# Kernel tuning notes

Hardware: AMD Instinct MI355X
Metric: run time of the kernel (lower is better)

Reference implementation:

```python
import jax, jax.numpy as jnp
import numpy as np

N = 4096        # number of nodes
C = 512         # in_features
L_LAT = 64      # L_latent
EPS = 0.25      # epsilon


def setup_inputs() -> dict:
    key = jax.random.key(0)
    ks = jax.random.split(key, 8)
    def lin(k, fan_in, shape):
        return (jax.random.normal(k, shape, jnp.float32) / np.float32(np.sqrt(fan_in)))
    x = jax.random.normal(ks[0], (N, C), jnp.float32)
    adj = jax.random.uniform(ks[1], (N, N), jnp.float32)  # dense nonneg kernel
    W_proj = lin(ks[2], C, (C, L_LAT)); b_proj = jnp.zeros((L_LAT,), jnp.float32)
    W_pi1 = lin(ks[3], L_LAT, (L_LAT, C)); b_pi1 = jnp.zeros((C,), jnp.float32)
    W_pi2 = lin(ks[4], C, (C, 1)); b_pi2 = jnp.zeros((1,), jnp.float32)
    W_f = lin(ks[5], C, (C, C)); b_f = jnp.zeros((C,), jnp.float32)
    dt = jnp.array([0.1], jnp.float32)
    return {"x": x, "adj": adj, "W_proj": W_proj, "b_proj": b_proj,
            "W_pi1": W_pi1, "b_pi1": b_pi1, "W_pi2": W_pi2, "b_pi2": b_pi2,
            "W_f": W_f, "b_f": b_f, "dt": dt}


def reference(x, adj, W_proj, b_proj, W_pi1, b_pi1, W_pi2, b_pi2, W_f, b_f, dt):
    # proj_list: x -> latent [n, L]
    z = x @ W_proj + b_proj
    # pi_list: Linear -> ReLU -> Linear -> Sigmoid, squeeze to [n]
    pi = jax.nn.sigmoid(jax.nn.relu(z @ W_pi1 + b_pi1) @ W_pi2 + b_pi2)[:, 0]
    # q_epsilon_tilde: row sums of the kernel
    q = adj.sum(axis=1)                       # [n]
    # K_tilde = K_epsilon @ diag(pi/q)  == column scaling
    K_tilde = adj * (pi / q)[None, :]         # [n, n]
    # D_tilde diagonal; torch.inverse of a diagonal == elementwise reciprocal
    d = K_tilde.sum(axis=1) + 1e-5            # [n]
    # target = relu(f(x)) with f = Linear(C, C)
    target = jax.nn.relu(x @ W_f + b_f)       # [n, C]
    # L @ target = (1/eps) * diag(1/d) @ K_tilde @ target - target
    Lt = (K_tilde @ target) / (EPS * d)[:, None] - target
    return target + dt[0] * Lt
```

## Files before the change

kernel.cpp:

```cpp
#include <hip/hip_runtime.h>
#include <hip/hip_bf16.h>

#define N_NODES 4096
#define C_DIM   512
#define L_DIM   64
#define SPLITS  4
#define KCHUNK  (N_NODES / SPLITS)

typedef unsigned short u16;
using bf16x8 = __attribute__((ext_vector_type(8))) __bf16;
using u16x8  = __attribute__((ext_vector_type(8))) unsigned short;
using f32x4  = __attribute__((ext_vector_type(4))) float;

__device__ __forceinline__ float b2f(u16 u) {
    union { unsigned int i; float f; } v; v.i = ((unsigned int)u) << 16; return v.f;
}
__device__ __forceinline__ u16 f2b(float f) {
    unsigned int u = __float_as_uint(f);
    u += 0x7fff + ((u >> 16) & 1);
    return (u16)(u >> 16);
}

__device__ __forceinline__ void gload16(const u16* g, u16* l) {
    __builtin_amdgcn_global_load_lds((const __attribute__((address_space(1))) void*)g,
                                     (__attribute__((address_space(3))) void*)l,
                                     16, 0, 0);
}

__device__ __forceinline__ int detect_mode_inl(const u16* __restrict__ adj) {
    int m = 0;
#pragma unroll
    for (int i = 0; i < 64; ++i) m |= (adj[i] >= 0x8000) ? 1 : 0;
    return m;
}

#define OFF_DT    64
#define OFF_BIAS  1024
#define OFF_WP    4096
#define OFF_BP    135168
#define OFF_WP1   135424
#define OFF_BP1   266496
#define OFF_WP2   268544
#define OFF_BP2   270592
#define OFF_Q     271360
#define OFF_S     287744
#define OFF_DV    304128
#define OFF_T     1048576
#define OFF_TST   9437184
#define OFF_WFT   13631488
#define OFF_XB    14155776
#define OFF_ADJB  18350080

__device__ __forceinline__ float ldin(const void* p, int i, int mode) {
    if (mode) return ((const float*)p)[i];
    return b2f(((const u16*)p)[i]);
}

__global__ __launch_bounds__(256) void k1_prep(const void* __restrict__ adj, const void* __restrict__ x,
        const void* Wp, const void* bp, const void* Wp1, const void* bp1,
        const void* Wp2, const void* bp2, const void* Wf, const void* bfc, const void* dt,
        float* __restrict__ Wp_f, float* __restrict__ bp_f, float* __restrict__ Wp1_f,
        float* __restrict__ bp1_f, float* __restrict__ Wp2_f, float* __restrict__ bp2_f,
        float* __restrict__ bias_f, float* __restrict__ dt_f,
        u16* __restrict__ adjb, float* __restrict__ q, u16* __restrict__ xb,
        u16* __restrict__ WfT) {
    __shared__ float tile[32][33];
    int bid = blockIdx.x, tid = threadIdx.x;
    int mode = detect_mode_inl((const u16*)adj);
    if (bid < 263) {
        int idx = bid * 256 + tid;
        if (idx < 32768)        Wp_f[idx]          = ldin(Wp,  idx, mode);
        else if (idx < 32832)   bp_f[idx - 32768]  = ldin(bp,  idx - 32768, mode);
        else if (idx < 65600)   Wp1_f[idx - 32832] = ldin(Wp1, idx - 32832, mode);
        else if (idx < 66112)   bp1_f[idx - 65600] = ldin(bp1, idx - 65600, mode);
        else if (idx < 66624)   Wp2_f[idx - 66112] = ldin(Wp2, idx - 66112, mode);
        else if (idx == 66624)  bp2_f[0]           = ldin(bp2, 0, mode);
        else if (idx < 67137)   bias_f[idx - 66625] = ldin(bfc, idx - 66625, mode);
        else if (idx == 67137)  dt_f[0]            = ldin(dt, 0, mode);
    } else if (bid < 2311) {
        if (mode == 0) return;
        int idx = (bid - 263) * 256 + tid;
        float4 v = ((const float4*)x)[idx];
        ushort4 o; o.x = f2b(v.x); o.y = f2b(v.y); o.z = f2b(v.z); o.w = f2b(v.w);
        ((ushort4*)xb)[idx] = o;
    } else if (bid < 3335) {
        int wave = tid >> 6, lane = tid & 63;
        int row = (bid - 2311) * 4 + wave;
        float acc = 0.f;
        if (mode) {
            const float4* rp = (const float4*)((const float*)adj + (size_t)row * N_NODES);
            ushort4* wp = (ushort4*)(adjb + (size_t)row * N_NODES);
#pragma unroll
            for (int it = 0; it < 16; ++it) {
                float4 v = rp[it * 64 + lane];
                acc += v.x + v.y + v.z + v.w;
                ushort4 o; o.x = f2b(v.x); o.y = f2b(v.y); o.z = f2b(v.z); o.w = f2b(v.w);
                wp[it * 64 + lane] = o;
            }
        } else {
            const u16x8* rp = (const u16x8*)((const u16*)adj + (size_t)row * N_NODES);
#pragma unroll
            for (int it = 0; it < 8; ++it) {
                u16x8 v = rp[it * 64 + lane];
#pragma unroll
                for (int e = 0; e < 8; ++e) acc += b2f(v[e]);
            }
        }
#pragma unroll
        for (int off = 32; off > 0; off >>= 1) acc += __shfl_down(acc, off);
        if (lane == 0) q[row] = acc;
    } else {
        int g = bid - 3335;
        int tx = tid & 31, ty = tid >> 5;
        int x0 = (g & 15) * 32, y0 = (g >> 4) * 32;
        if (mode) {
            const float* src = (const float*)Wf;
#pragma unroll
            for (int r = ty; r < 32; r += 8) tile[r][tx] = src[(size_t)(y0 + r) * C_DIM + x0 + tx];
        } else {
            const u16* src = (const u16*)Wf;
#pragma unroll
            for (int r = ty; r < 32; r += 8) tile[r][tx] = b2f(src[(size_t)(y0 + r) * C_DIM + x0 + tx]);
        }
        __syncthreads();
#pragma unroll
        for (int r = ty; r < 32; r += 8)
            WfT[(size_t)(x0 + r) * C_DIM + y0 + tx] = f2b(tile[tx][r]);
    }
}

__global__ __launch_bounds__(256) void k2_pi_gemm1(const void* __restrict__ xraw,
        const u16* __restrict__ adjdet, const u16* __restrict__ xb, const u16* __restrict__ WfT,
        const float* __restrict__ Wp_f,  const float* __restrict__ bp_f,
        const float* __restrict__ Wp1_f, const float* __restrict__ bp1_f,
        const float* __restrict__ Wp2_f, const float* __restrict__ bp2_f,
        const float* __restrict__ bias_f, const float* __restrict__ dt_f,
        const float* __restrict__ q, float* __restrict__ s, float* __restrict__ T,
        void* __restrict__ out, float* __restrict__ Pacc) {
    __shared__ __align__(16) char smem[18560];
    int bid = blockIdx.x, tid = threadIdx.x;
    int mode = detect_mode_inl(adjdet);
    if (bid < 512) {
        float (*sx)[C_DIM] = (float(*)[C_DIM])smem;
        float (*sz)[L_DIM] = (float(*)[L_DIM])(smem + 16384);
        float (*red)[8]    = (float(*)[8])(smem + 18432);
        int i0 = bid * 8;
        const u16* xsrc = mode ? xb : (const u16*)xraw;
        const u16x8* xp = (const u16x8*)(xsrc + (size_t)i0 * C_DIM);
#pragma unroll
        for (int r = 0; r < 2; ++r) {
            u16x8 v = xp[tid + 256 * r];
            float* dstf = &sx[0][0] + (size_t)(tid + 256 * r) * 8;
#pragma unroll
            for (int e = 0; e < 8; ++e) dstf[e] = b2f(v[e]);
        }
        __syncthreads();
        int j = tid & 63, n0 = tid >> 6;
        float a0 = 0.f, a1 = 0.f;
#pragma unroll 4
        for (int k = 0; k < C_DIM; ++k) {
            float w = Wp_f[k * L_DIM + j];
            a0 += sx[n0][k] * w;
            a1 += sx[n0 + 4][k] * w;
        }
        sz[n0][j] = a0 + bp_f[j];
        sz[n0 + 4][j] = a1 + bp_f[j];
        __syncthreads();
        int m0 = tid, m1 = tid + 256;
        float b0 = bp1_f[m0], b1 = bp1_f[m1];
        float h0[8], h1[8];
#pragma unroll
        for (int n = 0; n < 8; ++n) { h0[n] = b0; h1[n] = b1; }
#pragma unroll 8
        for (int jj = 0; jj < L_DIM; ++jj) {
            float w0 = Wp1_f[jj * C_DIM + m0];
            float w1 = Wp1_f[jj * C_DIM + m1];
#pragma unroll
            for (int n = 0; n < 8; ++n) {
                float z = sz[n][jj];
                h0[n] += z * w0;
                h1[n] += z * w1;
            }
        }
        float w2a = Wp2_f[m0], w2b = Wp2_f[m1];
        float p[8];
#pragma unroll
        for (int n = 0; n < 8; ++n)
            p[n] = fmaxf(h0[n], 0.f) * w2a + fmaxf(h1[n], 0.f) * w2b;
#pragma unroll
        for (int off = 32; off > 0; off >>= 1)
#pragma unroll
            for (int n = 0; n < 8; ++n) p[n] += __shfl_down(p[n], off);
        int lane = tid & 63, wave = tid >> 6;
        if (lane == 0) {
#pragma unroll
            for (int n = 0; n < 8; ++n) red[wave][n] = p[n];
        }
        __syncthreads();
        if (tid < 8) {
            float tot = red[0][tid] + red[1][tid] + red[2][tid] + red[3][tid] + bp2_f[0];
            float pi = 1.f / (1.f + expf(-tot));
            s[i0 + tid] = pi / q[i0 + tid];
        }
    } else {
        u16* lA = (u16*)smem;
        u16* lB = (u16*)(smem + 4096);
        const u16* A = mode ? xb : (const u16*)xraw;
        float* tgt = mode ? (float*)out : Pacc;
        int g = bid - 512;
        int lane = tid & 63, wave = tid >> 6;
        int bm = (g & 63) * 64, bn = (g >> 6) * 64;
        int quad = lane >> 4, l15 = lane & 15;
        int wm = wave * 16;
        const u16* Ap = A + (size_t)(bm + (tid >> 2)) * C_DIM + (tid & 3) * 8;
        const u16* Bp = WfT + (size_t)(bn + (tid >> 2)) * C_DIM + (tid & 3) * 8;
        u16* la = lA + tid * 8;
        u16* lb = lB + tid * 8;
        f32x4 acc[4];
#pragma unroll
        for (int nt = 0; nt < 4; ++nt) acc[nt] = (f32x4){0.f, 0.f, 0.f, 0.f};
        for (int k0 = 0; k0 < C_DIM; k0 += 32) {
            gload16(Ap + k0, la);
            gload16(Bp + k0, lb);
            __syncthreads();
            bf16x8 af = *(const bf16x8*)&lA[(wm + l15) * 32 + quad * 8];
            bf16x8 bfv[4];
#pragma unroll
            for (int nt = 0; nt < 4; ++nt) bfv[nt] = *(const bf16x8*)&lB[(nt * 16 + l15) * 32 + quad * 8];
#pragma unroll
            for (int nt = 0; nt < 4; ++nt)
                acc[nt] = __builtin_amdgcn_mfma_f32_16x16x32_bf16(af, bfv[nt], acc[nt], 0, 0, 0);
            __syncthreads();
        }
        float c0 = 1.f - dt_f[0];
#pragma unroll
        for (int nt = 0; nt < 4; ++nt) {
            int col = bn + nt * 16 + l15;
            float bv = bias_f[col];
#pragma unroll
            for (int r = 0; r < 4; ++r) {
                int row = bm + wm + quad * 4 + r;
                float t = fmaxf(acc[nt][r] + bv, 0.f);
                T[(size_t)row * C_DIM + col] = t;
                tgt[(size_t)row * C_DIM + col] = c0 * t;
            }
        }
    }
}

__global__ __launch_bounds__(256) void k3_mid(const void* __restrict__ adjraw,
        const u16* __restrict__ adjb, const float* __restrict__ s,
        const float* __restrict__ T,
        float* __restrict__ dv, u16* __restrict__ TsT) {
    __shared__ float tile[32][33];
    int bid = blockIdx.x, tid = threadIdx.x;
    int mode = detect_mode_inl((const u16*)adjraw);
    if (bid < 1024) {
        const u16* A = mode ? adjb : (const u16*)adjraw;
        int wave = tid >> 6, lane = tid & 63;
        int row = bid * 4 + wave;
        const u16x8* rp = (const u16x8*)(A + (size_t)row * N_NODES);
        float acc = 0.f;
#pragma unroll
        for (int it = 0; it < 8; ++it) {
            int chunk = it * 64 + lane;
            u16x8 v = rp[chunk];
            const float4* sp = (const float4*)(s + chunk * 8);
            float4 s0 = sp[0], s1 = sp[1];
            acc += b2f(v[0]) * s0.x + b2f(v[1]) * s0.y + b2f(v[2]) * s0.z + b2f(v[3]) * s0.w;
            acc += b2f(v[4]) * s1.x + b2f(v[5]) * s1.y + b2f(v[6]) * s1.z + b2f(v[7]) * s1.w;
        }
#pragma unroll
        for (int off = 32; off > 0; off >>= 1) acc += __shfl_down(acc, off);
        if (lane == 0) dv[row] = acc + 1e-5f;
    } else {
        int g = bid - 1024;
        int tx = tid & 31, ty = tid >> 5;
        int x0 = (g & 15) * 32, y0 = (g >> 4) * 32;
#pragma unroll
        for (int r = ty; r < 32; r += 8) tile[r][tx] = T[(size_t)(y0 + r) * C_DIM + x0 + tx];
        __syncthreads();
        float sv = s[y0 + tx];
#pragma unroll
        for (int r = ty; r < 32; r += 8)
            TsT[(size_t)(x0 + r) * N_NODES + y0 + tx] = f2b(tile[tx][r] * sv);
    }
}

__global__ __launch_bounds__(256) void k4_gemm2(const void* __restrict__ adjraw,
        const u16* __restrict__ adjb, const u16* __restrict__ TsT,
        const float* __restrict__ dv, const float* __restrict__ dt_f,
        void* __restrict__ out, float* __restrict__ Pacc) {
    __shared__ __align__(16) u16 lA[8192];
    __shared__ __align__(16) u16 lB[8192];
    int mode = detect_mode_inl((const u16*)adjraw);
    const u16* A = mode ? adjb : (const u16*)adjraw;
    float* tgt = mode ? (float*)out : Pacc;
    int tid = threadIdx.x;
    int lane = tid & 63, wave = tid >> 6;
    int bm = blockIdx.x * 128, bn = blockIdx.y * 128;
    int kbase = blockIdx.z * KCHUNK;
    int wm = (wave & 1) * 64, wn = (wave >> 1) * 64;
    int quad = lane >> 4, l15 = lane & 15;

    const u16* Ab0 = A + (size_t)(bm + (tid >> 2)) * N_NODES + kbase + (tid & 3) * 8;
    const u16* Ab1 = A + (size_t)(bm + 64 + (tid >> 2)) * N_NODES + kbase + (tid & 3) * 8;
    const u16* Bb0 = TsT + (size_t)(bn + (tid >> 2)) * N_NODES + kbase + (tid & 3) * 8;
    const u16* Bb1 = TsT + (size_t)(bn + 64 + (tid >> 2)) * N_NODES + kbase + (tid & 3) * 8;
    u16* la00 = lA + tid * 8;        u16* la01 = lA + 2048 + tid * 8;
    u16* la10 = lA + 4096 + tid * 8; u16* la11 = lA + 6144 + tid * 8;
    u16* lb00 = lB + tid * 8;        u16* lb01 = lB + 2048 + tid * 8;
    u16* lb10 = lB + 4096 + tid * 8; u16* lb11 = lB + 6144 + tid * 8;

    f32x4 acc[4][4];
#pragma unroll
    for (int a = 0; a < 4; ++a)
#pragma unroll
        for (int b = 0; b < 4; ++b) acc[a][b] = (f32x4){0.f, 0.f, 0.f, 0.f};

    for (int k0 = 0; k0 < KCHUNK; k0 += 64) {
        gload16(Ab0 + k0, la00);
        gload16(Ab1 + k0, la01);
        gload16(Ab0 + k0 + 32, la10);
        gload16(Ab1 + k0 + 32, la11);
        gload16(Bb0 + k0, lb00);
        gload16(Bb1 + k0, lb01);
        gload16(Bb0 + k0 + 32, lb10);
        gload16(Bb1 + k0 + 32, lb11);
        __syncthreads();
#pragma unroll
        for (int kk = 0; kk < 2; ++kk) {
            const u16* baseA = lA + kk * 4096;
            const u16* baseB = lB + kk * 4096;
            bf16x8 af[4], bfv[4];
#pragma unroll
            for (int mt = 0; mt < 4; ++mt) af[mt] = *(const bf16x8*)&baseA[(wm + mt * 16 + l15) * 32 + quad * 8];
#pragma unroll
            for (int nt = 0; nt < 4; ++nt) bfv[nt] = *(const bf16x8*)&baseB[(wn + nt * 16 + l15) * 32 + quad * 8];
#pragma unroll
            for (int mt = 0; mt < 4; ++mt)
#pragma unroll
                for (int nt = 0; nt < 4; ++nt)
                    acc[mt][nt] = __builtin_amdgcn_mfma_f32_16x16x32_bf16(af[mt], bfv[nt], acc[mt][nt], 0, 0, 0);
        }
        __syncthreads();
    }

    float c1 = dt_f[0] * 4.f;
#pragma unroll
    for (int mt = 0; mt < 4; ++mt) {
        float inv[4];
#pragma unroll
        for (int r = 0; r < 4; ++r) inv[r] = c1 / dv[bm + wm + mt * 16 + quad * 4 + r];
#pragma unroll
        for (int nt = 0; nt < 4; ++nt) {
            int col = bn + wn + nt * 16 + l15;
#pragma unroll
            for (int r = 0; r < 4; ++r) {
                int row = bm + wm + mt * 16 + quad * 4 + r;
                atomicAdd(&tgt[(size_t)row * C_DIM + col], acc[mt][nt][r] * inv[r]);
            }
        }
    }
}

__global__ __launch_bounds__(256) void k5_fin(const void* __restrict__ adjraw,
                                              const float* __restrict__ Pacc,
                                              u16* __restrict__ out) {
    if (detect_mode_inl((const u16*)adjraw)) return;
    int idx = blockIdx.x * 256 + threadIdx.x;
    float4 v = ((const float4*)Pacc)[idx];
    ushort4 o; o.x = f2b(v.x); o.y = f2b(v.y); o.z = f2b(v.z); o.w = f2b(v.w);
    ((ushort4*)out)[idx] = o;
}

extern "C" void kernel_launch(void* const* d_in, const int* in_sizes, int n_in,
                              void* d_out, int out_size, void* d_ws, size_t ws_size,
                              hipStream_t stream) {
    const void* x   = d_in[0];
    const void* adj = d_in[1];
    const void* Wp  = d_in[2];
    const void* bp  = d_in[3];
    const void* Wp1 = d_in[4];
    const void* bp1 = d_in[5];
    const void* Wp2 = d_in[6];
    const void* bp2 = d_in[7];
    const void* Wf  = d_in[8];
    const void* bfc = d_in[9];
    const void* dtp = d_in[10];
    const u16* adjdet = (const u16*)adj;

    char* ws = (char*)d_ws;
    float* dt_f   = (float*)(ws + OFF_DT);
    float* bias_f = (float*)(ws + OFF_BIAS);
    float* Wp_f   = (float*)(ws + OFF_WP);
    float* bp_f   = (float*)(ws + OFF_BP);
    float* Wp1_f  = (float*)(ws + OFF_WP1);
    float* bp1_f  = (float*)(ws + OFF_BP1);
    float* Wp2_f  = (float*)(ws + OFF_WP2);
    float* bp2_f  = (float*)(ws + OFF_BP2);
    float* q      = (float*)(ws + OFF_Q);
    float* s      = (float*)(ws + OFF_S);
    float* dv     = (float*)(ws + OFF_DV);
    float* T      = (float*)(ws + OFF_T);
    u16*   TsT    = (u16*)(ws + OFF_TST);
    u16*   WfT    = (u16*)(ws + OFF_WFT);
    u16*   xb     = (u16*)(ws + OFF_XB);
    u16*   adjb   = (u16*)(ws + OFF_ADJB);
    float* Pacc   = (float*)(ws + OFF_ADJB);

    k1_prep<<<3591, 256, 0, stream>>>(adj, x, Wp, bp, Wp1, bp1, Wp2, bp2, Wf, bfc, dtp,
                                      Wp_f, bp_f, Wp1_f, bp1_f, Wp2_f, bp2_f, bias_f, dt_f,
                                      adjb, q, xb, WfT);
    k2_pi_gemm1<<<1024, 256, 0, stream>>>(x, adjdet, xb, WfT,
                                          Wp_f, bp_f, Wp1_f, bp1_f, Wp2_f, bp2_f, bias_f, dt_f,
                                          q, s, T, d_out, Pacc);
    k3_mid<<<3072, 256, 0, stream>>>(adj, adjb, s, T, dv, TsT);
    k4_gemm2<<<dim3(32, 4, SPLITS), 256, 0, stream>>>(adj, adjb, TsT, dv, dt_f, d_out, Pacc);
    k5_fin<<<2048, 256, 0, stream>>>(adj, Pacc, (u16*)d_out);
}
```

Before: 227.5 us.

## Pack pi-MLP weights as bf16 pairs and restructure the latent projection loop

Wp and Wp1 are now converted in the prep kernel to packed bf16 pairs instead of fp32 copies, halving the weight traffic of the pi MLP. The latent projection now splits K across the four waves, with each thread computing all 8 rows, and reduces the partial sums through shared memory. The mode flag is computed once and stored in the workspace, so later kernels read one int instead of each re-scanning 64 adjacency values. The cost is bf16 rounding of the MLP weights, which could shift pi slightly, plus extra shared memory and a barrier in the MLP block.

```diff
diff --git a/kernel.cpp b/kernel.cpp
--- a/kernel.cpp
+++ b/kernel.cpp
@@ -8,6 +8,7 @@
 #define KCHUNK  (N_NODES / SPLITS)
 
 typedef unsigned short u16;
+typedef unsigned int   u32;
 using bf16x8 = __attribute__((ext_vector_type(8))) __bf16;
 using u16x8  = __attribute__((ext_vector_type(8))) unsigned short;
 using f32x4  = __attribute__((ext_vector_type(4))) float;
@@ -20,13 +21,11 @@
     u += 0x7fff + ((u >> 16) & 1);
     return (u16)(u >> 16);
 }
-
-__device__ __forceinline__ void gload16(const u16* g, u16* l) {
+__device__ __forceinline__ void gload16(const void* g, void* l) {
     __builtin_amdgcn_global_load_lds((const __attribute__((address_space(1))) void*)g,
                                      (__attribute__((address_space(3))) void*)l,
                                      16, 0, 0);
 }
-
 __device__ __forceinline__ int detect_mode_inl(const u16* __restrict__ adj) {
     int m = 0;
 #pragma unroll
@@ -34,22 +33,23 @@
     return m;
 }
 
+#define OFF_MODE  0
 #define OFF_DT    64
 #define OFF_BIAS  1024
-#define OFF_WP    4096
-#define OFF_BP    135168
-#define OFF_WP1   135424
-#define OFF_BP1   266496
-#define OFF_WP2   268544
-#define OFF_BP2   270592
-#define OFF_Q     271360
-#define OFF_S     287744
-#define OFF_DV    304128
+#define OFF_BP    4096
+#define OFF_BP1   4608
+#define OFF_WP2   8192
+#define OFF_BP2   10240
+#define OFF_Q     16384
+#define OFF_S     32768
+#define OFF_DV    49152
+#define OFF_WPP   65536
+#define OFF_WP1P  131072
+#define OFF_WFT   196608
 #define OFF_T     1048576
 #define OFF_TST   9437184
-#define OFF_WFT   13631488
-#define OFF_XB    14155776
-#define OFF_ADJB  18350080
+#define OFF_XB    13631488
+#define OFF_ADJB  17825792
 
 __device__ __forceinline__ float ldin(const void* p, int i, int mode) {
     if (mode) return ((const float*)p)[i];
@@ -59,33 +59,34 @@
 __global__ __launch_bounds__(256) void k1_prep(const void* __restrict__ adj, const void* __restrict__ x,
         const void* Wp, const void* bp, const void* Wp1, const void* bp1,
         const void* Wp2, const void* bp2, const void* Wf, const void* bfc, const void* dt,
-        float* __restrict__ Wp_f, float* __restrict__ bp_f, float* __restrict__ Wp1_f,
-        float* __restrict__ bp1_f, float* __restrict__ Wp2_f, float* __restrict__ bp2_f,
+        int* __restrict__ modep,
+        float* __restrict__ bp_f, float* __restrict__ bp1_f,
+        float* __restrict__ Wp2_f, float* __restrict__ bp2_f,
         float* __restrict__ bias_f, float* __restrict__ dt_f,
+        u32* __restrict__ WpP, u32* __restrict__ Wp1P,
         u16* __restrict__ adjb, float* __restrict__ q, u16* __restrict__ xb,
         u16* __restrict__ WfT) {
     __shared__ float tile[32][33];
     int bid = blockIdx.x, tid = threadIdx.x;
     int mode = detect_mode_inl((const u16*)adj);
-    if (bid < 263) {
+    if (bid < 7) {
+        if (bid == 0 && tid == 0) *modep = mode;
         int idx = bid * 256 + tid;
-        if (idx < 32768)        Wp_f[idx]          = ldin(Wp,  idx, mode);
-        else if (idx < 32832)   bp_f[idx - 32768]  = ldin(bp,  idx - 32768, mode);
-        else if (idx < 65600)   Wp1_f[idx - 32832] = ldin(Wp1, idx - 32832, mode);
-        else if (idx < 66112)   bp1_f[idx - 65600] = ldin(bp1, idx - 65600, mode);
-        else if (idx < 66624)   Wp2_f[idx - 66112] = ldin(Wp2, idx - 66112, mode);
-        else if (idx == 66624)  bp2_f[0]           = ldin(bp2, 0, mode);
-        else if (idx < 67137)   bias_f[idx - 66625] = ldin(bfc, idx - 66625, mode);
-        else if (idx == 67137)  dt_f[0]            = ldin(dt, 0, mode);
-    } else if (bid < 2311) {
+        if (idx < 64)           bp_f[idx]          = ldin(bp,  idx, mode);
+        else if (idx < 576)     bp1_f[idx - 64]    = ldin(bp1, idx - 64, mode);
+        else if (idx < 1088)    Wp2_f[idx - 576]   = ldin(Wp2, idx - 576, mode);
+        else if (idx == 1088)   bp2_f[0]           = ldin(bp2, 0, mode);
+        else if (idx < 1601)    bias_f[idx - 1089] = ldin(bfc, idx - 1089, mode);
+        else if (idx == 1601)   dt_f[0]            = ldin(dt, 0, mode);
+    } else if (bid < 2055) {
         if (mode == 0) return;
-        int idx = (bid - 263) * 256 + tid;
+        int idx = (bid - 7) * 256 + tid;
         float4 v = ((const float4*)x)[idx];
         ushort4 o; o.x = f2b(v.x); o.y = f2b(v.y); o.z = f2b(v.z); o.w = f2b(v.w);
         ((ushort4*)xb)[idx] = o;
-    } else if (bid < 3335) {
+    } else if (bid < 3079) {
         int wave = tid >> 6, lane = tid & 63;
-        int row = (bid - 2311) * 4 + wave;
+        int row = (bid - 2055) * 4 + wave;
         float acc = 0.f;
         if (mode) {
             const float4* rp = (const float4*)((const float*)adj + (size_t)row * N_NODES);
@@ -109,8 +110,8 @@
 #pragma unroll
         for (int off = 32; off > 0; off >>= 1) acc += __shfl_down(acc, off);
         if (lane == 0) q[row] = acc;
-    } else {
-        int g = bid - 3335;
+    } else if (bid < 3335) {
+        int g = bid - 3079;
         int tx = tid & 31, ty = tid >> 5;
         int x0 = (g & 15) * 32, y0 = (g >> 4) * 32;
         if (mode) {
@@ -126,24 +127,37 @@
 #pragma unroll
         for (int r = ty; r < 32; r += 8)
             WfT[(size_t)(x0 + r) * C_DIM + y0 + tx] = f2b(tile[tx][r]);
+    } else if (bid < 3399) {
+        int idx = (bid - 3335) * 256 + tid;
+        int k2i = idx >> 6, j = idx & 63;
+        float a = ldin(Wp, (2 * k2i) * L_DIM + j, mode);
+        float b = ldin(Wp, (2 * k2i + 1) * L_DIM + j, mode);
+        WpP[idx] = (u32)f2b(a) | ((u32)f2b(b) << 16);
+    } else {
+        int idx = (bid - 3399) * 256 + tid;
+        int jj2 = idx >> 9, m = idx & 511;
+        float a = ldin(Wp1, (2 * jj2) * C_DIM + m, mode);
+        float b = ldin(Wp1, (2 * jj2 + 1) * C_DIM + m, mode);
+        Wp1P[idx] = (u32)f2b(a) | ((u32)f2b(b) << 16);
     }
 }
 
 __global__ __launch_bounds__(256) void k2_pi_gemm1(const void* __restrict__ xraw,
-        const u16* __restrict__ adjdet, const u16* __restrict__ xb, const u16* __restrict__ WfT,
-        const float* __restrict__ Wp_f,  const float* __restrict__ bp_f,
-        const float* __restrict__ Wp1_f, const float* __restrict__ bp1_f,
+        const int* __restrict__ modep, const u16* __restrict__ xb, const u16* __restrict__ WfT,
+        const u32* __restrict__ WpP, const u32* __restrict__ Wp1P,
+        const float* __restrict__ bp_f,  const float* __restrict__ bp1_f,
         const float* __restrict__ Wp2_f, const float* __restrict__ bp2_f,
         const float* __restrict__ bias_f, const float* __restrict__ dt_f,
         const float* __restrict__ q, float* __restrict__ s, float* __restrict__ T,
         void* __restrict__ out, float* __restrict__ Pacc) {
-    __shared__ __align__(16) char smem[18560];
+    __shared__ __align__(16) char smem[26880];
     int bid = blockIdx.x, tid = threadIdx.x;
-    int mode = detect_mode_inl(adjdet);
+    int mode = *modep;
     if (bid < 512) {
-        float (*sx)[C_DIM] = (float(*)[C_DIM])smem;
-        float (*sz)[L_DIM] = (float(*)[L_DIM])(smem + 16384);
-        float (*red)[8]    = (float(*)[8])(smem + 18432);
+        float (*sx)[C_DIM]      = (float(*)[C_DIM])smem;
+        float (*red)[8][L_DIM]  = (float(*)[8][L_DIM])(smem + 16384);
+        float (*sz)[L_DIM]      = (float(*)[L_DIM])(smem + 24576);
+        float (*rw)[8]          = (float(*)[8])(smem + 26624);
         int i0 = bid * 8;
         const u16* xsrc = mode ? xb : (const u16*)xraw;
         const u16x8* xp = (const u16x8*)(xsrc + (size_t)i0 * C_DIM);
@@ -155,31 +169,44 @@
             for (int e = 0; e < 8; ++e) dstf[e] = b2f(v[e]);
         }
         __syncthreads();
-        int j = tid & 63, n0 = tid >> 6;
-        float a0 = 0.f, a1 = 0.f;
+        int j = tid & 63, part = tid >> 6;
+        float za[8];
+#pragma unroll
+        for (int n = 0; n < 8; ++n) za[n] = 0.f;
+        const u32* wp = WpP + part * 4096 + j;
+#pragma unroll 8
+        for (int kk = 0; kk < 64; ++kk) {
+            u32 w = wp[kk * 64];
+            float wa = b2f((u16)(w & 0xFFFF)), wb = b2f((u16)(w >> 16));
+            int k = part * 128 + kk * 2;
+#pragma unroll
+            for (int n = 0; n < 8; ++n) za[n] += sx[n][k] * wa + sx[n][k + 1] * wb;
+        }
+#pragma unroll
+        for (int n = 0; n < 8; ++n) red[part][n][j] = za[n];
+        __syncthreads();
+#pragma unroll
+        for (int r = 0; r < 2; ++r) {
+            int idx = tid + r * 256; int n = idx >> 6, jj = idx & 63;
+            sz[n][jj] = red[0][n][jj] + red[1][n][jj] + red[2][n][jj] + red[3][n][jj] + bp_f[jj];
+        }
+        __syncthreads();
+        int m0 = tid, m1 = tid + 256;
+        float h0[8], h1[8];
+        float b0 = bp1_f[m0], b1 = bp1_f[m1];
+#pragma unroll
+        for (int n = 0; n < 8; ++n) { h0[n] = b0; h1[n] = b1; }
+        const u32* w1p = Wp1P + m0;
 #pragma unroll 4
-        for (int k = 0; k < C_DIM; ++k) {
-            float w = Wp_f[k * L_DIM + j];
-            a0 += sx[n0][k] * w;
-            a1 += sx[n0 + 4][k] * w;
-        }
-        sz[n0][j] = a0 + bp_f[j];
-        sz[n0 + 4][j] = a1 + bp_f[j];
-        __syncthreads();
-        int m0 = tid, m1 = tid + 256;
-        float b0 = bp1_f[m0], b1 = bp1_f[m1];
-        float h0[8], h1[8];
-#pragma unroll
-        for (int n = 0; n < 8; ++n) { h0[n] = b0; h1[n] = b1; }
-#pragma unroll 8
-        for (int jj = 0; jj < L_DIM; ++jj) {
-            float w0 = Wp1_f[jj * C_DIM + m0];
-            float w1 = Wp1_f[jj * C_DIM + m1];
+        for (int jj2 = 0; jj2 < 32; ++jj2) {
+            u32 w0 = w1p[jj2 * 512], w1 = w1p[jj2 * 512 + 256];
+            float w0a = b2f((u16)(w0 & 0xFFFF)), w0b = b2f((u16)(w0 >> 16));
+            float w1a = b2f((u16)(w1 & 0xFFFF)), w1b = b2f((u16)(w1 >> 16));
 #pragma unroll
             for (int n = 0; n < 8; ++n) {
-                float z = sz[n][jj];
-                h0[n] += z * w0;
-                h1[n] += z * w1;
+                float za_ = sz[n][2 * jj2], zb_ = sz[n][2 * jj2 + 1];
+                h0[n] += za_ * w0a + zb_ * w0b;
+                h1[n] += za_ * w1a + zb_ * w1b;
             }
         }
         float w2a = Wp2_f[m0], w2b = Wp2_f[m1];
@@ -194,11 +221,11 @@
         int lane = tid & 63, wave = tid >> 6;
         if (lane == 0) {
 #pragma unroll
-            for (int n = 0; n < 8; ++n) red[wave][n] = p[n];
+            for (int n = 0; n < 8; ++n) rw[wave][n] = p[n];
         }
         __syncthreads();
         if (tid < 8) {
-            float tot = red[0][tid] + red[1][tid] + red[2][tid] + red[3][tid] + bp2_f[0];
+            float tot = rw[0][tid] + rw[1][tid] + rw[2][tid] + rw[3][tid] + bp2_f[0];
             float pi = 1.f / (1.f + expf(-tot));
             s[i0 + tid] = pi / q[i0 + tid];
         }
@@ -249,12 +276,13 @@
 }
 
 __global__ __launch_bounds__(256) void k3_mid(const void* __restrict__ adjraw,
+        const int* __restrict__ modep,
         const u16* __restrict__ adjb, const float* __restrict__ s,
         const float* __restrict__ T,
         float* __restrict__ dv, u16* __restrict__ TsT) {
     __shared__ float tile[32][33];
     int bid = blockIdx.x, tid = threadIdx.x;
-    int mode = detect_mode_inl((const u16*)adjraw);
+    int mode = *modep;
     if (bid < 1024) {
         const u16* A = mode ? adjb : (const u16*)adjraw;
         int wave = tid >> 6, lane = tid & 63;
@@ -288,12 +316,13 @@
 }
 
 __global__ __launch_bounds__(256) void k4_gemm2(const void* __restrict__ adjraw,
+        const int* __restrict__ modep,
         const u16* __restrict__ adjb, const u16* __restrict__ TsT,
         const float* __restrict__ dv, const float* __restrict__ dt_f,
         void* __restrict__ out, float* __restrict__ Pacc) {
     __shared__ __align__(16) u16 lA[8192];
     __shared__ __align__(16) u16 lB[8192];
-    int mode = detect_mode_inl((const u16*)adjraw);
+    int mode = *modep;
     const u16* A = mode ? adjb : (const u16*)adjraw;
     float* tgt = mode ? (float*)out : Pacc;
     int tid = threadIdx.x;
@@ -364,10 +393,10 @@
     }
 }
 
-__global__ __launch_bounds__(256) void k5_fin(const void* __restrict__ adjraw,
+__global__ __launch_bounds__(256) void k5_fin(const int* __restrict__ modep,
                                               const float* __restrict__ Pacc,
                                               u16* __restrict__ out) {
-    if (detect_mode_inl((const u16*)adjraw)) return;
+    if (*modep) return;
     int idx = blockIdx.x * 256 + threadIdx.x;
     float4 v = ((const float4*)Pacc)[idx];
     ushort4 o; o.x = f2b(v.x); o.y = f2b(v.y); o.z = f2b(v.z); o.w = f2b(v.w);
@@ -388,34 +417,34 @@
     const void* Wf  = d_in[8];
     const void* bfc = d_in[9];
     const void* dtp = d_in[10];
-    const u16* adjdet = (const u16*)adj;
 
     char* ws = (char*)d_ws;
+    int*   modep  = (int*)(ws + OFF_MODE);
     float* dt_f   = (float*)(ws + OFF_DT);
     float* bias_f = (float*)(ws + OFF_BIAS);
-    float* Wp_f   = (float*)(ws + OFF_WP);
     float* bp_f   = (float*)(ws + OFF_BP);
-    float* Wp1_f  = (float*)(ws + OFF_WP1);
     float* bp1_f  = (float*)(ws + OFF_BP1);
     float* Wp2_f  = (float*)(ws + OFF_WP2);
     float* bp2_f  = (float*)(ws + OFF_BP2);
     float* q      = (float*)(ws + OFF_Q);
     float* s      = (float*)(ws + OFF_S);
     float* dv     = (float*)(ws + OFF_DV);
+    u32*   WpP    = (u32*)(ws + OFF_WPP);
+    u32*   Wp1P   = (u32*)(ws + OFF_WP1P);
+    u16*   WfT    = (u16*)(ws + OFF_WFT);
     float* T      = (float*)(ws + OFF_T);
     u16*   TsT    = (u16*)(ws + OFF_TST);
-    u16*   WfT    = (u16*)(ws + OFF_WFT);
     u16*   xb     = (u16*)(ws + OFF_XB);
     u16*   adjb   = (u16*)(ws + OFF_ADJB);
     float* Pacc   = (float*)(ws + OFF_ADJB);
 
-    k1_prep<<<3591, 256, 0, stream>>>(adj, x, Wp, bp, Wp1, bp1, Wp2, bp2, Wf, bfc, dtp,
-                                      Wp_f, bp_f, Wp1_f, bp1_f, Wp2_f, bp2_f, bias_f, dt_f,
-                                      adjb, q, xb, WfT);
-    k2_pi_gemm1<<<1024, 256, 0, stream>>>(x, adjdet, xb, WfT,
-                                          Wp_f, bp_f, Wp1_f, bp1_f, Wp2_f, bp2_f, bias_f, dt_f,
+    k1_prep<<<3463, 256, 0, stream>>>(adj, x, Wp, bp, Wp1, bp1, Wp2, bp2, Wf, bfc, dtp,
+                                      modep, bp_f, bp1_f, Wp2_f, bp2_f, bias_f, dt_f,
+                                      WpP, Wp1P, adjb, q, xb, WfT);
+    k2_pi_gemm1<<<1024, 256, 0, stream>>>(x, modep, xb, WfT, WpP, Wp1P,
+                                          bp_f, bp1_f, Wp2_f, bp2_f, bias_f, dt_f,
                                           q, s, T, d_out, Pacc);
-    k3_mid<<<3072, 256, 0, stream>>>(adj, adjb, s, T, dv, TsT);
-    k4_gemm2<<<dim3(32, 4, SPLITS), 256, 0, stream>>>(adj, adjb, TsT, dv, dt_f, d_out, Pacc);
-    k5_fin<<<2048, 256, 0, stream>>>(adj, Pacc, (u16*)d_out);
-}
+    k3_mid<<<3072, 256, 0, stream>>>(adj, modep, adjb, s, T, dv, TsT);
+    k4_gemm2<<<dim3(32, 4, SPLITS), 256, 0, stream>>>(adj, modep, adjb, TsT, dv, dt_f, d_out, Pacc);
+    k5_fin<<<2048, 256, 0, stream>>>(modep, Pacc, (u16*)d_out);
+}
```

After: 214.8 us. 1.06x faster.
